# Performance work log

Hardware: AMD Instinct MI355X
Metric: run time of the kernel (lower is better)

## Reference

```python
import jax, jax.numpy as jnp
import numpy as np
import math

# Model dims (see shape_source)
N_EMBD = 2048
QK_H = 128      # per-head qk dim
V_H = 128       # per-head v dim
Q_DIM = N_EMBD                 # 2048 -> 16 query heads
N_HEAD = Q_DIM // QK_H         # 16
KV_HEAD = N_HEAD // 4          # 4 (GQA)
K_DIM = KV_HEAD * QK_H         # 512
V_DIM = KV_HEAD * V_H          # 512
D_KV = K_DIM + V_DIM           # 1024, S6 channel dim
D_STATE = 16                   # S6 state size
DT_RANK = math.ceil(D_KV / 16) # 'auto' -> 64
WINDOW = 512
B, T = 1, 4096


def setup_inputs() -> dict:
    key = jax.random.key(0)
    ks = jax.random.split(key, 8)
    x = jax.random.normal(ks[0], (B, T, N_EMBD), jnp.float32)
    W_attn = jax.random.normal(ks[1], (Q_DIM + K_DIM + V_DIM, N_EMBD), jnp.float32) * 0.02
    # S6 params (canonical Mamba S6 init: A = -exp(A_log), A_log = log(1..N))
    A_log = jnp.log(jnp.arange(1, D_STATE + 1, dtype=jnp.float32))[None, :] * jnp.ones((D_KV, 1), jnp.float32)
    x_proj_w = jax.random.normal(ks[2], (DT_RANK + 2 * D_STATE, D_KV), jnp.float32) * 0.02
    dt_proj_w = jax.random.normal(ks[3], (D_KV, DT_RANK), jnp.float32) * 0.02
    dt_proj_b = jax.random.normal(ks[4], (D_KV,), jnp.float32) * 0.1
    D_param = jnp.ones((D_KV,), jnp.float32)
    W_o = jax.random.normal(ks[5], (N_EMBD, Q_DIM), jnp.float32) * 0.02
    return dict(x=x, W_attn=W_attn, A_log=A_log, x_proj_w=x_proj_w,
                dt_proj_w=dt_proj_w, dt_proj_b=dt_proj_b, D_param=D_param,
                W_o=W_o, window_size=WINDOW)


def s6_scan(u, A_log, x_proj_w, dt_proj_w, dt_proj_b, D_param):
    """Canonical S6 selective scan. u: (B, T, D) -> (B, T, D)."""
    Bb, Tt, D = u.shape
    N = A_log.shape[1]
    dt_rank = dt_proj_w.shape[1]
    x_dbl = jnp.einsum('btd,ed->bte', u, x_proj_w)          # (B,T,dt_rank+2N)
    dt, Bm, Cm = jnp.split(x_dbl, [dt_rank, dt_rank + N], axis=-1)
    delta = jax.nn.softplus(jnp.einsum('btr,dr->btd', dt, dt_proj_w) + dt_proj_b)  # (B,T,D)
    A = -jnp.exp(A_log)                                      # (D,N), negative
    dA = jnp.exp(delta[..., None] * A)                       # (B,T,D,N)
    dBu = delta[..., None] * Bm[:, :, None, :] * u[..., None]  # (B,T,D,N)

    def step(h, inp):
        dA_t, dBu_t, C_t = inp
        h = dA_t * h + dBu_t                                 # (B,D,N)
        y = jnp.einsum('bdn,bn->bd', h, C_t)
        return h, y

    h0 = jnp.zeros((Bb, D, N), u.dtype)
    _, ys = jax.lax.scan(step, h0,
                         (dA.transpose(1, 0, 2, 3), dBu.transpose(1, 0, 2, 3), Cm.transpose(1, 0, 2)))
    y = ys.transpose(1, 0, 2)                                # (B,T,D)
    return y + D_param * u


def sliding_window_attn(q, k, v, window, scale):
    """Causal sliding-window attention; query i attends to j in [i-(window-1), i].
    q: (B,T,H,dh), k/v: (B,T,Hk,dh). Blockwise with one look-back block."""
    Bb, Tt, H, dh = q.shape
    Hk = k.shape[2]
    G = H // Hk
    k = jnp.repeat(k, G, axis=2)
    v = jnp.repeat(v, G, axis=2)
    W = window
    nb = Tt // W
    # (B,H,nb,W,dh)
    qb = q.reshape(Bb, nb, W, H, dh).transpose(0, 3, 1, 2, 4)
    kb = k.reshape(Bb, nb, W, H, dh).transpose(0, 3, 1, 2, 4)
    vb = v.reshape(Bb, nb, W, H, dh).transpose(0, 3, 1, 2, 4)
    # previous block (zeros for first block)
    kprev = jnp.pad(kb, ((0, 0), (0, 0), (1, 0), (0, 0), (0, 0)))[:, :, :nb]
    vprev = jnp.pad(vb, ((0, 0), (0, 0), (1, 0), (0, 0), (0, 0)))[:, :, :nb]
    k2 = jnp.concatenate([kprev, kb], axis=3)                # (B,H,nb,2W,dh)
    v2 = jnp.concatenate([vprev, vb], axis=3)
    scores = jnp.einsum('bhwid,bhwjd->bhwij', qb * scale, k2)  # (B,H,nb,W,2W)
    i = jnp.arange(W)[:, None]
    j = jnp.arange(2 * W)[None, :]
    rel = i + W - j                                          # absolute i - j
    base_mask = (rel >= 0) & (rel <= W - 1)                  # causal & within window
    blk = jnp.arange(nb)[:, None, None]
    valid = base_mask[None] & ((j[None] >= W) | (blk > 0))   # first block: no look-back
    neg = jnp.finfo(jnp.float32).max
    scores = jnp.where(valid[None, None], scores, -neg)
    attn = jax.nn.softmax(scores.astype(jnp.float32), axis=-1).astype(q.dtype)
    out = jnp.einsum('bhwij,bhwjd->bhwid', attn, v2)         # (B,H,nb,W,dh)
    return out.transpose(0, 2, 3, 1, 4).reshape(Bb, Tt, H, dh)


def reference(x, W_attn, A_log, x_proj_w, dt_proj_w, dt_proj_b, D_param, W_o, window_size):
    Bb, Tt, C = x.shape
    qkv = jnp.einsum('btc,oc->bto', x, W_attn)
    q = qkv[..., :Q_DIM]
    kv = qkv[..., Q_DIM:]
    kv = s6_scan(kv, A_log, x_proj_w, dt_proj_w, dt_proj_b, D_param)
    k = kv[..., :K_DIM]
    v = kv[..., K_DIM:]
    q = q.reshape(Bb, Tt, N_HEAD, QK_H)
    k = k.reshape(Bb, Tt, KV_HEAD, QK_H)
    v = v.reshape(Bb, Tt, KV_HEAD, V_H)
    scale = 1.0 / math.sqrt(QK_H)
    y = sliding_window_attn(q, k, v, window_size, scale)     # (B,T,H,v_h)
    y = y.reshape(Bb, Tt, -1)
    return jnp.einsum('bto,no->btn', y, W_o)
```

## Files before the change

### kernel.cpp

```cpp
#include <hip/hip_runtime.h>
#include <hip/hip_bf16.h>

typedef __hip_bfloat16 bf16;
typedef __attribute__((ext_vector_type(8))) short bf16x8;
typedef __attribute__((ext_vector_type(4))) float f32x4;

#define T_SEQ 4096
#define NEMBD 2048
#define QKVD  3072
#define QDIM  2048
#define DKV   1024
#define KDIM  512
#define NH    16
#define DH    128
#define NST   16
#define DTR   64
#define WIN   512
#define NCHUNK 64
#define CLEN   64

__device__ inline float bf2f(bf16 x) { return __bfloat162float(x); }

struct F8 { float v[8]; };

__device__ inline F8 load_b8(const bf16* p) {
  union { uint4 q; unsigned short s[8]; } u;
  u.q = *reinterpret_cast<const uint4*>(p);
  F8 r;
#pragma unroll
  for (int i = 0; i < 8; i++) r.v[i] = __uint_as_float((unsigned)u.s[i] << 16);
  return r;
}

__device__ inline F8 load8(const void* base, size_t idx, int f32flag) {
  if (f32flag) {
    const float4* p = reinterpret_cast<const float4*>((const float*)base + idx);
    float4 a = p[0], b = p[1];
    F8 r;
    r.v[0]=a.x; r.v[1]=a.y; r.v[2]=a.z; r.v[3]=a.w;
    r.v[4]=b.x; r.v[5]=b.y; r.v[6]=b.z; r.v[7]=b.w;
    return r;
  }
  return load_b8((const bf16*)base + idx);
}

__device__ inline float load1(const void* base, size_t idx, int f32flag) {
  return f32flag ? ((const float*)base)[idx] : bf2f(((const bf16*)base)[idx]);
}

__device__ inline unsigned short f2b_bits(float f) {
  bf16 h = __float2bfloat16(f);
  union { bf16 h; unsigned short u; } c; c.h = h; return c.u;
}

__device__ inline ushort4 pack4(float a, float b, float c, float d) {
  ushort4 r; r.x = f2b_bits(a); r.y = f2b_bits(b); r.z = f2b_bits(c); r.w = f2b_bits(d);
  return r;
}

__device__ inline void gld_lds16(const void* g, void* l) {
  __builtin_amdgcn_global_load_lds(
      (const __attribute__((address_space(1))) unsigned int*)g,
      (__attribute__((address_space(3))) unsigned int*)l, 16, 0, 0);
}

__global__ void detect_dtype(const unsigned short* __restrict__ x, int* __restrict__ flag) {
  if (threadIdx.x == 0 && blockIdx.x == 0) {
    int c = 0;
    for (int i = 0; i < 128; i++) {
      float v = __uint_as_float((unsigned)x[i] << 16);
      float a = fabsf(v);
      if (a >= 1e-8f && a <= 1e4f) c++;
    }
    flag[0] = (c >= 120) ? 0 : 1;
  }
}

#define N8_X   (T_SEQ * NEMBD / 8)
#define N8_WA  (QKVD * NEMBD / 8)
#define N8_WO  (NEMBD * QDIM / 8)
#define N8_XPW (96 * DKV / 8)
#define N8_DTW (DKV * DTR / 8)
#define N8_TOT (N8_X + N8_WA + N8_WO + N8_XPW + N8_DTW)

__global__ __launch_bounds__(256) void cvt_all(
    const void* __restrict__ x, const void* __restrict__ wa,
    const void* __restrict__ wo, const void* __restrict__ xpw,
    const void* __restrict__ dtw, const int* __restrict__ dflag,
    unsigned short* __restrict__ xo, unsigned short* __restrict__ wao,
    unsigned short* __restrict__ woo, unsigned short* __restrict__ xpwo,
    unsigned short* __restrict__ dtwo)
{
  int i = blockIdx.x * 256 + threadIdx.x;
  if (i >= N8_TOT) return;
  const int f = dflag[0];
  const void* in; unsigned short* out; size_t idx;
  if      (i < N8_X)                        { in = x;   out = xo;   idx = i; }
  else if (i < N8_X + N8_WA)                { in = wa;  out = wao;  idx = i - N8_X; }
  else if (i < N8_X + N8_WA + N8_WO)        { in = wo;  out = woo;  idx = i - (N8_X + N8_WA); }
  else if (i < N8_X + N8_WA + N8_WO + N8_XPW) { in = xpw; out = xpwo; idx = i - (N8_X + N8_WA + N8_WO); }
  else                                      { in = dtw; out = dtwo; idx = i - (N8_X + N8_WA + N8_WO + N8_XPW); }
  F8 v = load8(in, idx * 8, f);
  ushort4* o = (ushort4*)(out + idx * 8);
  o[0] = pack4(v.v[0], v.v[1], v.v[2], v.v[3]);
  o[1] = pack4(v.v[4], v.v[5], v.v[6], v.v[7]);
}

__global__ __launch_bounds__(512, 2) void gemm_wide(
    const unsigned short* __restrict__ A, const unsigned short* __restrict__ B,
    int M, int N, int K, int mode,
    bf16* __restrict__ oq, bf16* __restrict__ ou, float* __restrict__ oc)
{
  __shared__ unsigned short lds[2][384 * 64];
  const int tid = threadIdx.x;
  const int wave = tid >> 6, lane = tid & 63;
  const int quad = lane >> 4, l16 = lane & 15;
  const int wm = wave >> 1, wn = wave & 1;
  const int nbx = N >> 7;
  const int nwg = gridDim.x;
  const int chunk = nwg >> 3;
  const int swz = (blockIdx.x & 7) * chunk + (blockIdx.x >> 3);
  const int bm = (swz / nbx) * 256, bn = (swz % nbx) * 128;

  const int lrow = lane >> 3;
  const int lslot = (lane & 7) ^ lrow;
  const unsigned short* Abase = A + (size_t)(bm + wave * 8 + lrow) * K + lslot * 8;
  const unsigned short* Bbase = B + (size_t)(bn + wave * 8 + lrow) * K + lslot * 8;

  const int x7 = l16 & 7;
  const int s0 = ((0 + quad) ^ x7) * 8;
  const int s1 = ((4 + quad) ^ x7) * 8;
  const int arow0 = (wm * 64 + l16) * 64;
  const int brow0 = (256 + wn * 64 + l16) * 64;

  f32x4 acc[4][4];
#pragma unroll
  for (int i = 0; i < 4; i++)
#pragma unroll
    for (int j = 0; j < 4; j++) acc[i][j] = f32x4{0.f, 0.f, 0.f, 0.f};

  const int NT = K >> 6;

#pragma unroll
  for (int grp = 0; grp < 4; grp++)
    gld_lds16(Abase + (size_t)grp * 64 * K, &lds[0][(grp * 64 + wave * 8) * 64]);
#pragma unroll
  for (int grp = 0; grp < 2; grp++)
    gld_lds16(Bbase + (size_t)grp * 64 * K, &lds[0][(256 + grp * 64 + wave * 8) * 64]);
#pragma unroll
  for (int grp = 0; grp < 4; grp++)
    gld_lds16(Abase + (size_t)grp * 64 * K + 64, &lds[1][(grp * 64 + wave * 8) * 64]);
#pragma unroll
  for (int grp = 0; grp < 2; grp++)
    gld_lds16(Bbase + (size_t)grp * 64 * K + 64, &lds[1][(256 + grp * 64 + wave * 8) * 64]);
  asm volatile("s_waitcnt vmcnt(6)" ::: "memory");
  __builtin_amdgcn_sched_barrier(0);
  __builtin_amdgcn_s_barrier();

#define MM(m, n) \
  acc[m][n] = __builtin_amdgcn_mfma_f32_16x16x32_bf16(aF[m][0], bF[n][0], acc[m][n], 0, 0, 0); \
  acc[m][n] = __builtin_amdgcn_mfma_f32_16x16x32_bf16(aF[m][1], bF[n][1], acc[m][n], 0, 0, 0);

  for (int g = 0; g < NT; ++g) {
    const unsigned short* L = lds[g & 1];
    unsigned short* Lw = (unsigned short*)L;
    const bool stF = (g + 2) < NT;
    const size_t kF = (size_t)(g + 2) * 64;

    bf16x8 aF[4][2], bF[4][2];

#pragma unroll
    for (int m = 0; m < 4; m++) {
      aF[m][0] = *(const bf16x8*)&L[arow0 + m * 1024 + s0];
      aF[m][1] = *(const bf16x8*)&L[arow0 + m * 1024 + s1];
    }
    bF[0][0] = *(const bf16x8*)&L[brow0 +    0 + s0];
    bF[0][1] = *(const bf16x8*)&L[brow0 +    0 + s1];
    bF[1][0] = *(const bf16x8*)&L[brow0 + 1024 + s0];
    bF[1][1] = *(const bf16x8*)&L[brow0 + 1024 + s1];
    __builtin_amdgcn_s_barrier();
    if (stF) {
#pragma unroll
      for (int grp = 0; grp < 4; grp++)
        gld_lds16(Abase + (size_t)grp * 64 * K + kF, &Lw[(grp * 64 + wave * 8) * 64]);
    }
    __builtin_amdgcn_s_setprio(1);
    MM(0,0); MM(0,1); MM(1,0); MM(1,1);
    MM(2,0); MM(2,1); MM(3,0); MM(3,1);
    __builtin_amdgcn_s_setprio(0);
    __builtin_amdgcn_s_barrier();

    bF[2][0] = *(const bf16x8*)&L[brow0 + 2048 + s0];
    bF[2][1] = *(const bf16x8*)&L[brow0 + 2048 + s1];
    bF[3][0] = *(const bf16x8*)&L[brow0 + 3072 + s0];
    bF[3][1] = *(const bf16x8*)&L[brow0 + 3072 + s1];
    __builtin_amdgcn_s_barrier();
    if (stF) {
#pragma unroll
      for (int grp = 0; grp < 2; grp++)
        gld_lds16(Bbase + (size_t)grp * 64 * K + kF, &Lw[(256 + grp * 64 + wave * 8) * 64]);
    }
    __builtin_amdgcn_s_setprio(1);
    MM(0,2); MM(0,3); MM(1,2); MM(1,3);
    MM(2,2); MM(2,3); MM(3,2); MM(3,3);
    __builtin_amdgcn_s_setprio(0);
    if (stF) { asm volatile("s_waitcnt vmcnt(6)" ::: "memory"); }
    else     { asm volatile("s_waitcnt vmcnt(0)" ::: "memory"); }
    __builtin_amdgcn_sched_barrier(0);
    __builtin_amdgcn_s_barrier();
  }
#undef MM

#pragma unroll
  for (int m = 0; m < 4; m++)
#pragma unroll
    for (int n = 0; n < 4; n++) {
      int gm0 = bm + wm * 64 + m * 16 + quad * 4;
      int gn  = bn + wn * 64 + n * 16 + l16;
#pragma unroll
      for (int r = 0; r < 4; r++) {
        int gm = gm0 + r;
        float v = acc[m][n][r];
        if (mode == 0) {
          if (gn < QDIM) oq[(size_t)gm * QDIM + gn] = __float2bfloat16(v);
          else           ou[(size_t)gm * DKV + (gn - QDIM)] = __float2bfloat16(v);
        } else {
          oc[(size_t)gm * N + gn] = v;
        }
      }
    }
}

__global__ __launch_bounds__(256) void xdbl_mfma(
    const bf16* __restrict__ u, const unsigned short* __restrict__ xpw_bf,
    float* __restrict__ xd)
{
  __shared__ unsigned short Us[64 * 32];
  __shared__ unsigned short Ws[96 * 32];
  const int tid = threadIdx.x;
  const int wave = tid >> 6, lane = tid & 63;
  const int quad = lane >> 4, l16 = lane & 15;
  const int t0 = blockIdx.x * 64;
  const unsigned short* ub = (const unsigned short*)u;

  f32x4 acc[6];
#pragma unroll
  for (int j = 0; j < 6; j++) acc[j] = f32x4{0.f, 0.f, 0.f, 0.f};

  const int urow = tid >> 2, ucol = (tid & 3) * 8;
  const int wrow0 = tid >> 2, wcol0 = (tid & 3) * 8;
  const int wrow1 = (256 + tid) >> 2;

  uint4 upre = *(const uint4*)(ub + (size_t)(t0 + urow) * DKV + ucol);
  uint4 wpre0 = *(const uint4*)(xpw_bf + (size_t)wrow0 * DKV + wcol0);
  uint4 wpre1 = (tid < 128) ? *(const uint4*)(xpw_bf + (size_t)wrow1 * DKV + wcol0)
                            : uint4{0, 0, 0, 0};

  for (int k0 = 0; k0 < DKV; k0 += 32) {
    __syncthreads();
    *(uint4*)&Us[urow * 32 + ucol] = upre;
    *(uint4*)&Ws[wrow0 * 32 + wcol0] = wpre0;
    if (tid < 128) *(uint4*)&Ws[wrow1 * 32 + wcol0] = wpre1;
    __syncthreads();

    int kn = (k0 + 32 < DKV) ? (k0 + 32) : k0;
    upre  = *(const uint4*)(ub + (size_t)(t0 + urow) * DKV + kn + ucol);
    wpre0 = *(const uint4*)(xpw_bf + (size_t)wrow0 * DKV + kn + wcol0);
    if (tid < 128) wpre1 = *(const uint4*)(xpw_bf + (size_t)wrow1 * DKV + kn + wcol0);

    bf16x8 a = *(const bf16x8*)&Us[(wave * 16 + l16) * 32 + quad * 8];
#pragma unroll
    for (int j = 0; j < 6; j++) {
      bf16x8 b = *(const bf16x8*)&Ws[(j * 16 + l16) * 32 + quad * 8];
      acc[j] = __builtin_amdgcn_mfma_f32_16x16x32_bf16(a, b, acc[j], 0, 0, 0);
    }
  }

#pragma unroll
  for (int j = 0; j < 6; j++)
#pragma unroll
    for (int r = 0; r < 4; r++) {
      int t = t0 + wave * 16 + quad * 4 + r;
      xd[(size_t)t * 96 + j * 16 + l16] = acc[j][r];
    }
}

__global__ __launch_bounds__(256) void delta_mfma(
    const float* __restrict__ xd, const unsigned short* __restrict__ dtw_bf,
    const void* __restrict__ dtb, const int* __restrict__ dflag,
    bf16* __restrict__ delta)
{
  __shared__ unsigned short Xs[64 * 72];
  __shared__ unsigned short Ws[128 * 72];
  const int tid = threadIdx.x;
  const int wave = tid >> 6, lane = tid & 63;
  const int quad = lane >> 4, l16 = lane & 15;
  const int t0 = blockIdx.y * 64, d0 = blockIdx.x * 128;

  for (int e = tid; e < 64 * 8; e += 256) {
    int row = e >> 3, c8 = (e & 7) * 8;
    const float* p = xd + (size_t)(t0 + row) * 96 + c8;
    float4 a = *(const float4*)p, b = *(const float4*)(p + 4);
    *(ushort4*)&Xs[row * 72 + c8]     = pack4(a.x, a.y, a.z, a.w);
    *(ushort4*)&Xs[row * 72 + c8 + 4] = pack4(b.x, b.y, b.z, b.w);
  }
  for (int e = tid; e < 128 * 8; e += 256) {
    int row = e >> 3, c8 = (e & 7) * 8;
    *(uint4*)&Ws[row * 72 + c8] = *(const uint4*)(dtw_bf + (size_t)(d0 + row) * DTR + c8);
  }
  __syncthreads();

  bf16x8 a0 = *(const bf16x8*)&Xs[(wave * 16 + l16) * 72 + quad * 8];
  bf16x8 a1 = *(const bf16x8*)&Xs[(wave * 16 + l16) * 72 + 32 + quad * 8];

  f32x4 acc[8];
#pragma unroll
  for (int j = 0; j < 8; j++) {
    bf16x8 b0 = *(const bf16x8*)&Ws[(j * 16 + l16) * 72 + quad * 8];
    bf16x8 b1 = *(const bf16x8*)&Ws[(j * 16 + l16) * 72 + 32 + quad * 8];
    acc[j] = __builtin_amdgcn_mfma_f32_16x16x32_bf16(a0, b0, f32x4{0.f, 0.f, 0.f, 0.f}, 0, 0, 0);
    acc[j] = __builtin_amdgcn_mfma_f32_16x16x32_bf16(a1, b1, acc[j], 0, 0, 0);
  }

  const int f = dflag[0];
#pragma unroll
  for (int j = 0; j < 8; j++) {
    int d = d0 + j * 16 + l16;
    float bias = load1(dtb, d, f);
#pragma unroll
    for (int r = 0; r < 4; r++) {
      int t = t0 + wave * 16 + quad * 4 + r;
      float v = acc[j][r] + bias;
      float sp = fmaxf(v, 0.f) + log1pf(expf(-fabsf(v)));
      delta[(size_t)t * DKV + d] = __float2bfloat16(sp);
    }
  }
}

__global__ __launch_bounds__(256) void scan_pass1(
    const bf16* __restrict__ delta, const bf16* __restrict__ u,
    const float* __restrict__ xd, const void* __restrict__ A_log,
    const int* __restrict__ dflag, float* __restrict__ Pb, float* __restrict__ Hl)
{
  const int gid = blockIdx.x * 256 + threadIdx.x;
  const int c = gid >> 14;
  const int r = gid & 16383;
  const int d = r >> 4, n = r & 15;
  const int f = dflag[0];
  const float A = -expf(load1(A_log, d * NST + n, f));
  float p = 1.f, h = 0.f;
  const int t0 = c * CLEN;
  for (int tt = 0; tt < CLEN; tt++) {
    int t = t0 + tt;
    float dl = bf2f(delta[(size_t)t * DKV + d]);
    float uu = bf2f(u[(size_t)t * DKV + d]);
    float bm = xd[(size_t)t * 96 + DTR + n];
    float a = expf(dl * A);
    h = a * h + dl * bm * uu;
    p *= a;
  }
  Pb[gid] = p;
  Hl[gid] = h;
}

__global__ __launch_bounds__(256) void scan_combine(
    float* __restrict__ Pb, const float* __restrict__ Hl)
{
  const int idx = blockIdx.x * 256 + threadIdx.x;
  float run = 0.f;
  for (int c = 0; c < NCHUNK; c++) {
    size_t off = (size_t)c * 16384 + idx;
    float p = Pb[off], hl = Hl[off];
    Pb[off] = run;
    run = p * run + hl;
  }
}

__global__ __launch_bounds__(256) void scan_pass2(
    const bf16* __restrict__ delta, bf16* __restrict__ u,
    const float* __restrict__ xd, const void* __restrict__ A_log,
    const void* __restrict__ Dp, const int* __restrict__ dflag,
    const float* __restrict__ Hin, unsigned short* __restrict__ vt)
{
  __shared__ unsigned short vtile[16][72];
  const int gid = blockIdx.x * 256 + threadIdx.x;
  const int c = gid >> 14;
  const int r = gid & 16383;
  const int d = r >> 4, n = r & 15;
  const int dblk = ((int)(blockIdx.x & 63)) * 16;
  const bool isV = (dblk >= KDIM);
  const int f = dflag[0];
  const float A = -expf(load1(A_log, d * NST + n, f));
  const float dpar = load1(Dp, d, f);
  float h = Hin[gid];
  const int t0 = c * CLEN;
  for (int tt = 0; tt < CLEN; tt++) {
    int t = t0 + tt;
    float dl = bf2f(delta[(size_t)t * DKV + d]);
    float uu = bf2f(u[(size_t)t * DKV + d]);
    float bm = xd[(size_t)t * 96 + DTR + n];
    float cm = xd[(size_t)t * 96 + DTR + NST + n];
    float a = expf(dl * A);
    h = a * h + dl * bm * uu;
    float part = h * cm;
    part += __shfl_xor(part, 1);
    part += __shfl_xor(part, 2);
    part += __shfl_xor(part, 4);
    part += __shfl_xor(part, 8);
    if (n == 0) {
      float outv = part + dpar * uu;
      if (isV) vtile[d & 15][tt] = f2b_bits(outv);
      else     u[(size_t)t * DKV + d] = __float2bfloat16(outv);
    }
  }
  if (isV) {
    __syncthreads();
    const int tid = threadIdx.x;
    const int row = tid >> 4, c4 = (tid & 15) * 4;
    ushort4 w;
    w.x = vtile[row][c4];     w.y = vtile[row][c4 + 1];
    w.z = vtile[row][c4 + 2]; w.w = vtile[row][c4 + 3];
    *(ushort4*)&vt[(size_t)(dblk - KDIM + row) * T_SEQ + t0 + c4] = w;
  }
}

__global__ __launch_bounds__(256, 4) void attn_mfma(
    const bf16* __restrict__ q, const bf16* __restrict__ kv,
    const unsigned short* __restrict__ vt, bf16* __restrict__ y)
{
  __shared__ unsigned short Ks[32 * 136];
  __shared__ unsigned short Vts[128 * 40];
  __shared__ unsigned short Ps[4][16 * 40];
  const int tid = threadIdx.x;
  const int wave = tid >> 6, lane = tid & 63;
  const int quad = lane >> 4, l16 = lane & 15;
  const int qt = blockIdx.x, h = blockIdx.y, kvh = h >> 2;
  const int t0 = qt * 64;
  const float scale = 0.088388347648318447f;

  bf16x8 af[4];
#pragma unroll
  for (int s = 0; s < 4; s++)
    af[s] = *(const bf16x8*)(q + (size_t)(t0 + wave * 16 + l16) * QDIM
                             + h * DH + s * 32 + quad * 8);

  const int krow = tid >> 4, kc8 = (tid & 15) * 8;
  const int vrow = tid >> 2, vc8 = (tid & 3) * 8;
  const bf16* kgp = kv + (size_t)kvh * DH;
  const unsigned short* vgp = vt + (size_t)(kvh * DH) * T_SEQ;

  float m_r[4], l_p[4];
  f32x4 O[8];
#pragma unroll
  for (int r = 0; r < 4; r++) { m_r[r] = -1e30f; l_p[r] = 0.f; }
#pragma unroll
  for (int dt = 0; dt < 8; dt++) O[dt] = f32x4{0.f, 0.f, 0.f, 0.f};

  const int kb_start = (t0 > WIN - 1) ? ((t0 - (WIN - 1)) >> 5) : 0;
  const int kb_end = (t0 + 63) >> 5;

  uint4 kp0, kp1, vp0, vp1;
  {
    const int kb = kb_start;
    kp0 = *(const uint4*)(kgp + (size_t)(kb * 32 + krow) * DKV + kc8);
    kp1 = *(const uint4*)(kgp + (size_t)(kb * 32 + 16 + krow) * DKV + kc8);
    vp0 = *(const uint4*)(vgp + (size_t)vrow * T_SEQ + kb * 32 + vc8);
    vp1 = *(const uint4*)(vgp + (size_t)(vrow + 64) * T_SEQ + kb * 32 + vc8);
  }

  for (int kb = kb_start; kb <= kb_end; kb++) {
    __syncthreads();
    *(uint4*)&Ks[krow * 136 + kc8]        = kp0;
    *(uint4*)&Ks[(krow + 16) * 136 + kc8] = kp1;
    *(uint4*)&Vts[vrow * 40 + vc8]        = vp0;
    *(uint4*)&Vts[(vrow + 64) * 40 + vc8] = vp1;
    __syncthreads();

    if (kb < kb_end) {
      const int kn = kb + 1;
      kp0 = *(const uint4*)(kgp + (size_t)(kn * 32 + krow) * DKV + kc8);
      kp1 = *(const uint4*)(kgp + (size_t)(kn * 32 + 16 + krow) * DKV + kc8);
      vp0 = *(const uint4*)(vgp + (size_t)vrow * T_SEQ + kn * 32 + vc8);
      vp1 = *(const uint4*)(vgp + (size_t)(vrow + 64) * T_SEQ + kn * 32 + vc8);
    }

    f32x4 S0 = f32x4{0.f, 0.f, 0.f, 0.f}, S1 = f32x4{0.f, 0.f, 0.f, 0.f};
    __builtin_amdgcn_s_setprio(1);
#pragma unroll
    for (int s = 0; s < 4; s++) {
      bf16x8 b0 = *(const bf16x8*)&Ks[(l16) * 136 + s * 32 + quad * 8];
      bf16x8 b1 = *(const bf16x8*)&Ks[(16 + l16) * 136 + s * 32 + quad * 8];
      S0 = __builtin_amdgcn_mfma_f32_16x16x32_bf16(af[s], b0, S0, 0, 0, 0);
      S1 = __builtin_amdgcn_mfma_f32_16x16x32_bf16(af[s], b1, S1, 0, 0, 0);
    }
    __builtin_amdgcn_s_setprio(0);

    const int ka0 = kb * 32 + l16;
    const int ka1 = ka0 + 16;
    const bool full = (kb * 32 >= t0 + 63 - (WIN - 1)) && (kb * 32 + 31 <= t0);

    float v0r[4], v1r[4];
    bool x0r[4], x1r[4];
    bool ok = true;
#pragma unroll
    for (int r = 0; r < 4; r++) {
      int qa = t0 + wave * 16 + quad * 4 + r;
      float v0 = S0[r] * scale, v1 = S1[r] * scale;
      bool x0 = true, x1 = true;
      if (!full) {
        x0 = (ka0 <= qa) && (ka0 > qa - WIN);
        x1 = (ka1 <= qa) && (ka1 > qa - WIN);
        if (!x0) v0 = -1e30f;
        if (!x1) v1 = -1e30f;
      }
      v0r[r] = v0; v1r[r] = v1; x0r[r] = x0; x1r[r] = x1;
      ok = ok && (fmaxf(v0, v1) <= m_r[r] + 8.f);
    }

    if (!__all((int)ok)) {
#pragma unroll
      for (int r = 0; r < 4; r++) {
        float rm = fmaxf(v0r[r], v1r[r]);
        rm = fmaxf(rm, __shfl_xor(rm, 1));
        rm = fmaxf(rm, __shfl_xor(rm, 2));
        rm = fmaxf(rm, __shfl_xor(rm, 4));
        rm = fmaxf(rm, __shfl_xor(rm, 8));
        float mnew = fmaxf(m_r[r], rm);
        float al = __expf(m_r[r] - mnew);
        m_r[r] = mnew;
        l_p[r] *= al;
#pragma unroll
        for (int dt = 0; dt < 8; dt++) O[dt][r] *= al;
      }
    }

#pragma unroll
    for (int r = 0; r < 4; r++) {
      float p0 = x0r[r] ? __expf(v0r[r] - m_r[r]) : 0.f;
      float p1 = x1r[r] ? __expf(v1r[r] - m_r[r]) : 0.f;
      l_p[r] += p0 + p1;
      Ps[wave][(quad * 4 + r) * 40 + l16]      = f2b_bits(p0);
      Ps[wave][(quad * 4 + r) * 40 + 16 + l16] = f2b_bits(p1);
    }

    bf16x8 pa = *(const bf16x8*)&Ps[wave][l16 * 40 + quad * 8];
    __builtin_amdgcn_s_setprio(1);
#pragma unroll
    for (int dt = 0; dt < 8; dt++) {
      bf16x8 b = *(const bf16x8*)&Vts[(dt * 16 + l16) * 40 + quad * 8];
      O[dt] = __builtin_amdgcn_mfma_f32_16x16x32_bf16(pa, b, O[dt], 0, 0, 0);
    }
    __builtin_amdgcn_s_setprio(0);
  }

  float inv[4];
#pragma unroll
  for (int r = 0; r < 4; r++) {
    float l = l_p[r];
    l += __shfl_xor(l, 1);
    l += __shfl_xor(l, 2);
    l += __shfl_xor(l, 4);
    l += __shfl_xor(l, 8);
    inv[r] = 1.f / l;
  }
#pragma unroll
  for (int dt = 0; dt < 8; dt++)
#pragma unroll
    for (int r = 0; r < 4; r++) {
      int row = t0 + wave * 16 + quad * 4 + r;
      y[(size_t)row * QDIM + h * DH + dt * 16 + l16] = __float2bfloat16(O[dt][r] * inv[r]);
    }
}

extern "C" void kernel_launch(void* const* d_in, const int* in_sizes, int n_in,
                              void* d_out, int out_size, void* d_ws, size_t ws_size,
                              hipStream_t stream)
{
  const void* x      = d_in[0];
  const void* W_attn = d_in[1];
  const void* A_log  = d_in[2];
  const void* xpw    = d_in[3];
  const void* dtw    = d_in[4];
  const void* dtb    = d_in[5];
  const void* Dp     = d_in[6];
  const void* W_o    = d_in[7];

  char* ws = (char*)d_ws;
  int*   dflag = (int*)ws;   ws += 256;
  bf16*  u     = (bf16*)ws;  ws += (size_t)T_SEQ * DKV * 2;
  float* xd    = (float*)ws; ws += (size_t)T_SEQ * 96 * 4;
  char*  yreg  = ws;
  bf16*  delta = (bf16*)ws;  ws += (size_t)T_SEQ * DKV * 2;
  ws += (size_t)64 * DKV * NST * 4;
  ws += (size_t)64 * DKV * NST * 4;
  unsigned short* x_bf  = (unsigned short*)ws; ws += (size_t)T_SEQ * NEMBD * 2;
  unsigned short* wa_bf = (unsigned short*)ws; ws += (size_t)QKVD * NEMBD * 2;
  unsigned short* wo_bf = (unsigned short*)ws; ws += (size_t)NEMBD * QDIM * 2;
  unsigned short* vt    = (unsigned short*)ws; ws += (size_t)KDIM * T_SEQ * 2;
  unsigned short* xpw_bf = (unsigned short*)ws; ws += (size_t)96 * DKV * 2;
  unsigned short* dtw_bf = (unsigned short*)ws; ws += (size_t)DKV * DTR * 2;
  bf16*  y     = (bf16*)yreg;

  float* Pb = (float*)x_bf;
  float* Hl = Pb + (size_t)NCHUNK * DKV * NST;

  bf16*  q_bf = (bf16*)d_out;
  float* out  = (float*)d_out;

  detect_dtype<<<1, 64, 0, stream>>>((const unsigned short*)x, dflag);
  cvt_all<<<(N8_TOT + 255) / 256, 256, 0, stream>>>(
      x, W_attn, W_o, xpw, dtw, dflag, x_bf, wa_bf, wo_bf, xpw_bf, dtw_bf);

  gemm_wide<<<(T_SEQ / 256) * (QKVD / 128), 512, 0, stream>>>(
      x_bf, wa_bf, T_SEQ, QKVD, NEMBD, 0, q_bf, u, nullptr);
  xdbl_mfma<<<T_SEQ / 64, 256, 0, stream>>>(u, xpw_bf, xd);
  delta_mfma<<<dim3(DKV / 128, T_SEQ / 64), 256, 0, stream>>>(xd, dtw_bf, dtb, dflag, delta);
  scan_pass1<<<NCHUNK * 64, 256, 0, stream>>>(delta, u, xd, A_log, dflag, Pb, Hl);
  scan_combine<<<64, 256, 0, stream>>>(Pb, Hl);
  scan_pass2<<<NCHUNK * 64, 256, 0, stream>>>(delta, u, xd, A_log, Dp, dflag, Pb, vt);
  attn_mfma<<<dim3(T_SEQ / 64, NH), 256, 0, stream>>>(q_bf, u, vt, y);
  gemm_wide<<<(T_SEQ / 256) * (QDIM / 128), 512, 0, stream>>>(
      (const unsigned short*)y, wo_bf, T_SEQ, QDIM, QDIM, 1, nullptr, nullptr, out);
}
```

Baseline: 427.1 us.

## Split-K the x_proj GEMM and parallelize chunk-scan combine with warp shuffles

The x_dbl projection kernel now splits the 1024-wide reduction across four blocks per row tile and accumulates into a zeroed buffer with float atomics, raising the block count from 64 to 256. The scan_combine step, which walked 64 chunks serially with only 64 blocks, becomes a parallel Hillis-Steele scan over the (P, H) pairs using wave shuffles, with one wave per state channel. Both changes target low-occupancy serial phases. In exchange they add a memset launch and atomic traffic, and the floating-point summation order is no longer deterministic.

```diff
diff --git a/kernel.cpp b/kernel.cpp
--- a/kernel.cpp
+++ b/kernel.cpp
@@ -18,6 +18,7 @@
 #define WIN   512
 #define NCHUNK 64
 #define CLEN   64
+#define KSPLIT 4
 
 __device__ inline float bf2f(bf16 x) { return __bfloat162float(x); }
 
@@ -241,6 +242,8 @@
   const int wave = tid >> 6, lane = tid & 63;
   const int quad = lane >> 4, l16 = lane & 15;
   const int t0 = blockIdx.x * 64;
+  const int kbeg = blockIdx.y * (DKV / KSPLIT);
+  const int kend = kbeg + (DKV / KSPLIT);
   const unsigned short* ub = (const unsigned short*)u;
 
   f32x4 acc[6];
@@ -251,19 +254,19 @@
   const int wrow0 = tid >> 2, wcol0 = (tid & 3) * 8;
   const int wrow1 = (256 + tid) >> 2;
 
-  uint4 upre = *(const uint4*)(ub + (size_t)(t0 + urow) * DKV + ucol);
-  uint4 wpre0 = *(const uint4*)(xpw_bf + (size_t)wrow0 * DKV + wcol0);
-  uint4 wpre1 = (tid < 128) ? *(const uint4*)(xpw_bf + (size_t)wrow1 * DKV + wcol0)
+  uint4 upre = *(const uint4*)(ub + (size_t)(t0 + urow) * DKV + kbeg + ucol);
+  uint4 wpre0 = *(const uint4*)(xpw_bf + (size_t)wrow0 * DKV + kbeg + wcol0);
+  uint4 wpre1 = (tid < 128) ? *(const uint4*)(xpw_bf + (size_t)wrow1 * DKV + kbeg + wcol0)
                             : uint4{0, 0, 0, 0};
 
-  for (int k0 = 0; k0 < DKV; k0 += 32) {
+  for (int k0 = kbeg; k0 < kend; k0 += 32) {
     __syncthreads();
     *(uint4*)&Us[urow * 32 + ucol] = upre;
     *(uint4*)&Ws[wrow0 * 32 + wcol0] = wpre0;
     if (tid < 128) *(uint4*)&Ws[wrow1 * 32 + wcol0] = wpre1;
     __syncthreads();
 
-    int kn = (k0 + 32 < DKV) ? (k0 + 32) : k0;
+    int kn = (k0 + 32 < kend) ? (k0 + 32) : k0;
     upre  = *(const uint4*)(ub + (size_t)(t0 + urow) * DKV + kn + ucol);
     wpre0 = *(const uint4*)(xpw_bf + (size_t)wrow0 * DKV + kn + wcol0);
     if (tid < 128) wpre1 = *(const uint4*)(xpw_bf + (size_t)wrow1 * DKV + kn + wcol0);
@@ -281,7 +284,7 @@
 #pragma unroll
     for (int r = 0; r < 4; r++) {
       int t = t0 + wave * 16 + quad * 4 + r;
-      xd[(size_t)t * 96 + j * 16 + l16] = acc[j][r];
+      atomicAdd(&xd[(size_t)t * 96 + j * 16 + l16], acc[j][r]);
     }
 }
 
@@ -366,14 +369,18 @@
 __global__ __launch_bounds__(256) void scan_combine(
     float* __restrict__ Pb, const float* __restrict__ Hl)
 {
-  const int idx = blockIdx.x * 256 + threadIdx.x;
-  float run = 0.f;
-  for (int c = 0; c < NCHUNK; c++) {
-    size_t off = (size_t)c * 16384 + idx;
-    float p = Pb[off], hl = Hl[off];
-    Pb[off] = run;
-    run = p * run + hl;
-  }
+  const int idx = blockIdx.x * 4 + (threadIdx.x >> 6);
+  const int c = threadIdx.x & 63;
+  const size_t off = (size_t)c * 16384 + idx;
+  float P = Pb[off], H = Hl[off];
+#pragma unroll
+  for (int dstep = 1; dstep < 64; dstep <<= 1) {
+    float Pp = __shfl_up(P, dstep);
+    float Hp = __shfl_up(H, dstep);
+    if (c >= dstep) { H = P * Hp + H; P = P * Pp; }
+  }
+  float Hprev = __shfl_up(H, 1);
+  Pb[off] = (c == 0) ? 0.f : Hprev;
 }
 
 __global__ __launch_bounds__(256) void scan_pass2(
@@ -613,10 +620,11 @@
 
   gemm_wide<<<(T_SEQ / 256) * (QKVD / 128), 512, 0, stream>>>(
       x_bf, wa_bf, T_SEQ, QKVD, NEMBD, 0, q_bf, u, nullptr);
-  xdbl_mfma<<<T_SEQ / 64, 256, 0, stream>>>(u, xpw_bf, xd);
+  hipMemsetAsync(xd, 0, (size_t)T_SEQ * 96 * 4, stream);
+  xdbl_mfma<<<dim3(T_SEQ / 64, KSPLIT), 256, 0, stream>>>(u, xpw_bf, xd);
   delta_mfma<<<dim3(DKV / 128, T_SEQ / 64), 256, 0, stream>>>(xd, dtw_bf, dtb, dflag, delta);
   scan_pass1<<<NCHUNK * 64, 256, 0, stream>>>(delta, u, xd, A_log, dflag, Pb, Hl);
-  scan_combine<<<64, 256, 0, stream>>>(Pb, Hl);
+  scan_combine<<<16384 / 4, 256, 0, stream>>>(Pb, Hl);
   scan_pass2<<<NCHUNK * 64, 256, 0, stream>>>(delta, u, xd, A_log, Dp, dflag, Pb, vt);
   attn_mfma<<<dim3(T_SEQ / 64, NH), 256, 0, stream>>>(q_bf, u, vt, y);
   gemm_wide<<<(T_SEQ / 256) * (QDIM / 128), 512, 0, stream>>>(
```

New measurement: 437.2 us. 2.4% more time.
